# Performance work log

Hardware: AMD Instinct MI355X
Metric: run time of the kernel (lower is better)

## Reference

```python
import jax, jax.numpy as jnp
import numpy as np

N_EMBED = 1024
N_HEADS = 16
CTX = 2048
B, T = 4, 2048
HD = N_EMBED // N_HEADS


def setup_inputs() -> dict:
    key = jax.random.key(0)
    ks = jax.random.split(key, 5)
    scale = 1.0 / np.sqrt(N_EMBED)
    return {
        "x": jax.random.normal(ks[0], (B, T, N_EMBED), dtype=jnp.float32),
        "wq": jax.random.normal(ks[1], (N_EMBED, N_EMBED), dtype=jnp.float32) * scale,
        "wk": jax.random.normal(ks[2], (N_EMBED, N_EMBED), dtype=jnp.float32) * scale,
        "wv": jax.random.normal(ks[3], (N_EMBED, N_EMBED), dtype=jnp.float32) * scale,
        "wo": jax.random.normal(ks[4], (N_EMBED, N_EMBED), dtype=jnp.float32) * scale,
    }


def reference(x, wq, wk, wv, wo):
    b, t, c = x.shape
    # nn.Linear applies x @ W.T ; split heads -> [B, H, T, hd]
    def proj(w):
        return jnp.einsum("btc,dc->btd", x, w).reshape(b, t, N_HEADS, HD).transpose(0, 2, 1, 3)
    q, k, v = proj(wq), proj(wk), proj(wv)
    scores = jnp.einsum("bhqd,bhkd->bhqk", q, k) * (HD ** -0.5)
    causal = jnp.tril(jnp.ones((t, t), dtype=bool))
    scores = jnp.where(causal[None, None, :, :], scores, -jnp.inf)
    a = jax.nn.softmax(scores, axis=-1)
    o = jnp.einsum("bhqk,bhkd->bhqd", a, v)  # [B,H,T,hd]
    o = o.transpose(0, 2, 1, 3).reshape(b, t, c)
    return jnp.einsum("btc,dc->btd", o, wo)
```

## Files before the change

kernel.cpp:

```cpp
#include <hip/hip_runtime.h>
#include <stdint.h>


typedef __attribute__((ext_vector_type(8))) short bf16x8;
typedef __attribute__((ext_vector_type(4))) float f32x4;
typedef __attribute__((ext_vector_type(16))) float f32x16;
typedef unsigned short us;
typedef unsigned int u32;

#define LOG2E 1.4426950408889634f

#define GL2LDS16(g, l)                                                          \
  __builtin_amdgcn_global_load_lds(                                             \
      (const __attribute__((address_space(1))) unsigned int*)(g),               \
      (__attribute__((address_space(3))) unsigned int*)(l), 16, 0, 0)

__device__ inline us f2bf(float f) {
  union { float f; unsigned int u; } v; v.f = f;
  unsigned int u = v.u;
  u += 0x7FFFu + ((u >> 16) & 1u);
  return (us)(u >> 16);
}

__global__ void cast_all(const float* __restrict__ x,
                         const float* __restrict__ w0, const float* __restrict__ w1,
                         const float* __restrict__ w2, const float* __restrict__ w3,
                         us* __restrict__ xb, us* __restrict__ wbuf) {
  int i = (blockIdx.x * blockDim.x + threadIdx.x) * 8;
  const float* src;
  us* dst;
  float sc = 1.0f;
  if (i < (8 << 20)) {
    src = x + i; dst = xb + i;
  } else {
    int j = i - (8 << 20);
    int seg = j >> 20;
    int off = j & ((1 << 20) - 1);
    const float* w = (seg == 0) ? w0 : (seg == 1) ? w1 : (seg == 2) ? w2 : w3;
    if (seg == 0) sc = 0.125f * LOG2E;
    src = w + off; dst = wbuf + j;
  }
  float4 a = *reinterpret_cast<const float4*>(src);
  float4 b = *reinterpret_cast<const float4*>(src + 4);
  union { us u[8]; uint4 v; } o;
  o.u[0] = f2bf(a.x * sc); o.u[1] = f2bf(a.y * sc);
  o.u[2] = f2bf(a.z * sc); o.u[3] = f2bf(a.w * sc);
  o.u[4] = f2bf(b.x * sc); o.u[5] = f2bf(b.y * sc);
  o.u[6] = f2bf(b.z * sc); o.u[7] = f2bf(b.w * sc);
  *reinterpret_cast<uint4*>(dst) = o.v;
}

__global__ __launch_bounds__(512, 2) void gemm_qkv256(
    const us* __restrict__ A, const us* __restrict__ Bw,
    us* __restrict__ QKV, us* __restrict__ Vt) {
  const int K = 1024, N = 3072;
  __shared__ __align__(16) us As[4][8192];
  __shared__ __align__(16) us Bs[4][8192];
  const int tid = threadIdx.x;
  const int lane = tid & 63;
  const int w = tid >> 6;
  const int wm = w >> 2, wn = w & 3;
  const int quad = lane >> 4, l16 = lane & 15;

  const int bid = blockIdx.x;
  const int swz = (bid & 7) * 48 + (bid >> 3);
  const int mt = swz / 12, nt = swz % 12;
  const int m0 = mt * 256, n0 = nt * 256;

  const int j3 = (tid >> 3) & 7;
  const int upre = (tid & 7) ^ j3;
  const int Rb = ((tid >> 3) << 1) | (upre >> 2);
  const int kof = (upre & 3) * 8;
  const size_t arow0 = (size_t)(m0 + Rb) * K + kof;
  const size_t arow1 = (size_t)(m0 + Rb + 128) * K + kof;
  const size_t brow0 = (size_t)(n0 + Rb) * K + kof;
  const size_t brow1 = (size_t)(n0 + Rb + 128) * K + kof;
  const int wofs = __builtin_amdgcn_readfirstlane(w * 512);

  const int lrow = (l16 >> 1) * 64 +
                   ((((l16 & 1) * 4 + quad) ^ ((l16 >> 1) & 7)) * 8);

  f32x4 acc[8][4] = {};

  auto stage = [&](int ss, int ks) {
    const int sb = ss * 8192;
    GL2LDS16(A + arow0 + ks * 32, &As[0][sb + wofs]);
    GL2LDS16(A + arow1 + ks * 32, &As[0][sb + 4096 + wofs]);
    GL2LDS16(Bw + brow0 + ks * 32, &Bs[0][sb + wofs]);
    GL2LDS16(Bw + brow1 + ks * 32, &Bs[0][sb + 4096 + wofs]);
  };

  stage(0, 0);
  stage(1, 1);
  stage(2, 2);

#pragma unroll 1
  for (int s = 0; s < 32; ++s) {
    if (s < 29) {
      stage((s + 3) & 3, s + 3);
      asm volatile("s_waitcnt vmcnt(12)" ::: "memory");
    } else if (s == 29) {
      asm volatile("s_waitcnt vmcnt(8)" ::: "memory");
    } else if (s == 30) {
      asm volatile("s_waitcnt vmcnt(4)" ::: "memory");
    } else {
      asm volatile("s_waitcnt vmcnt(0)" ::: "memory");
    }
    asm volatile("s_barrier" ::: "memory");

    const int sb = (s & 3) * 8192;
    bf16x8 af[8], bf[4];
#pragma unroll
    for (int mi = 0; mi < 8; ++mi)
      af[mi] = *reinterpret_cast<const bf16x8*>(
          &As[0][sb + wm * 4096 + mi * 512 + lrow]);
#pragma unroll
    for (int ni = 0; ni < 4; ++ni)
      bf[ni] = *reinterpret_cast<const bf16x8*>(
          &Bs[0][sb + wn * 2048 + ni * 512 + lrow]);

    __builtin_amdgcn_s_setprio(1);
#pragma unroll
    for (int mi = 0; mi < 8; ++mi)
#pragma unroll
      for (int ni = 0; ni < 4; ++ni)
        acc[mi][ni] = __builtin_amdgcn_mfma_f32_16x16x32_bf16(af[mi], bf[ni], acc[mi][ni], 0, 0, 0);
    __builtin_amdgcn_s_setprio(0);

    asm volatile("s_barrier" ::: "memory");
  }

  if (n0 < 2048) {
#pragma unroll
    for (int mi = 0; mi < 8; ++mi)
#pragma unroll
      for (int ni = 0; ni < 4; ++ni)
#pragma unroll
        for (int r = 0; r < 4; ++r) {
          int row = m0 + wm * 128 + mi * 16 + quad * 4 + r;
          int col = n0 + wn * 64 + ni * 16 + l16;
          QKV[(size_t)row * N + col] = f2bf(acc[mi][ni][r]);
        }
  } else {
    const int bI = m0 >> 11;
    const int tbase = m0 & 2047;
#pragma unroll
    for (int mi = 0; mi < 8; ++mi)
#pragma unroll
      for (int ni = 0; ni < 4; ++ni)
#pragma unroll
        for (int r = 0; r < 4; ++r) {
          int krow = tbase + wm * 128 + mi * 16 + quad * 4 + r;
          int col = n0 + wn * 64 + ni * 16 + l16;
          int hh = (col - 2048) >> 6;
          int d = col & 63;
          Vt[((size_t)((bI * 16 + hh) * 64 + d)) * 2048 + krow] = f2bf(acc[mi][ni][r]);
        }
  }
}

__global__ __launch_bounds__(256, 2) void gemm_out(
    const us* __restrict__ A, const us* __restrict__ Bw,
    float* __restrict__ Cv, int M, int N, int K) {
  __shared__ __align__(16) us Al[128 * 64];
  __shared__ __align__(16) us Bl[128 * 64];
  const int tid = threadIdx.x;
  const int lane = tid & 63;
  const int w = tid >> 6;
  const int quad = lane >> 4;
  const int l16 = lane & 15;
  const int m0 = blockIdx.y * 128;
  const int n0 = blockIdx.x * 128;
  const int wm = w >> 1, wn = w & 1;
  const int srow_base = w * 8 + (lane >> 3);
  const int sunit = lane & 7;
  f32x4 acc[4][4] = {};

  for (int k0 = 0; k0 < K; k0 += 64) {
    __syncthreads();
#pragma unroll
    for (int it = 0; it < 4; ++it) {
      int row = it * 32 + srow_base;
      int gu = sunit ^ (row & 7);
      int base = __builtin_amdgcn_readfirstlane((it * 256 + w * 64) * 8);
      GL2LDS16(A + (size_t)(m0 + row) * K + k0 + gu * 8, &Al[base]);
      GL2LDS16(Bw + (size_t)(n0 + row) * K + k0 + gu * 8, &Bl[base]);
    }
    __syncthreads();
#pragma unroll
    for (int kk = 0; kk < 2; ++kk) {
      bf16x8 af[4], bfr[4];
#pragma unroll
      for (int mi = 0; mi < 4; ++mi) {
        int row = wm * 64 + mi * 16 + l16;
        af[mi] = *reinterpret_cast<const bf16x8*>(
            &Al[row * 64 + (((kk * 4 + quad) ^ (row & 7)) * 8)]);
      }
#pragma unroll
      for (int ni = 0; ni < 4; ++ni) {
        int row = wn * 64 + ni * 16 + l16;
        bfr[ni] = *reinterpret_cast<const bf16x8*>(
            &Bl[row * 64 + (((kk * 4 + quad) ^ (row & 7)) * 8)]);
      }
#pragma unroll
      for (int mi = 0; mi < 4; ++mi)
#pragma unroll
        for (int ni = 0; ni < 4; ++ni)
          acc[mi][ni] = __builtin_amdgcn_mfma_f32_16x16x32_bf16(af[mi], bfr[ni], acc[mi][ni], 0, 0, 0);
    }
  }

#pragma unroll
  for (int mi = 0; mi < 4; ++mi)
#pragma unroll
    for (int ni = 0; ni < 4; ++ni)
#pragma unroll
      for (int r = 0; r < 4; ++r) {
        int row = m0 + wm * 64 + mi * 16 + quad * 4 + r;
        int col = n0 + wn * 64 + ni * 16 + l16;
        Cv[(size_t)row * N + col] = acc[mi][ni][r];
      }
}

__global__ __launch_bounds__(256, 3) void attn(
    const us* __restrict__ QKV, const us* __restrict__ Vt,
    us* __restrict__ O) {
  __shared__ __align__(16) us Kb[2][64 * 64];
  __shared__ __align__(16) us Vb[2][64 * 64];
  __shared__ float Ls[4][32];
  const int bid = blockIdx.x;
  const int j16 = bid >> 6;
  const int grp = j16 >> 2, pos = j16 & 3;
  const int qt = (grp == 0) ? 15 - pos : (grp == 1) ? pos
               : (grp == 2) ? 11 - pos : 4 + pos;
  const int bh = bid & 63;
  const int b = bh >> 4, h = bh & 15;
  const int q0 = qt * 128;
  const int tid = threadIdx.x, lane = tid & 63, w = tid >> 6;
  const int l31 = lane & 31, hi = lane >> 5;
  const size_t rowbase = (size_t)b * 2048;
  const int qcol = h * 64;
  const int kcol = 1024 + h * 64;
  const int qw = q0 + w * 32;
  const int nT = 2 * qt + 2;

  const int mr = (l31 & 7) ^ ((l31 >> 3) & 3);

  bf16x8 qf[4];
#pragma unroll
  for (int ds = 0; ds < 4; ++ds)
    qf[ds] = *reinterpret_cast<const bf16x8*>(
        &QKV[(rowbase + qw + l31) * 3072 + qcol + ds * 16 + hi * 8]);

  f32x16 oacc[2] = {};
  float psum = 0.f;

  const int rr8 = w * 8 + (lane >> 3);
  const int ms = (rr8 & 7) ^ ((rr8 >> 3) & 3);
  const int uu = lane & 7;
  const int gu = uu ^ ms;

  auto stage = [&](int kt, int buf) {
#pragma unroll
    for (int c = 0; c < 2; ++c) {
      int row = c * 32 + rr8;
      int base = __builtin_amdgcn_readfirstlane((c * 32 + w * 8) * 64);
      GL2LDS16(QKV + (rowbase + kt * 64 + row) * 3072 + kcol + gu * 8,
               &Kb[buf][base]);
      GL2LDS16(Vt + ((size_t)(bh * 64 + row)) * 2048 + kt * 64 + gu * 8,
               &Vb[buf][base]);
    }
  };

  stage(0, 0);

  for (int kt = 0; kt < nT; ++kt) {
    asm volatile("s_waitcnt vmcnt(0)" ::: "memory");
    asm volatile("s_barrier" ::: "memory");
    if (kt + 1 < nT) stage(kt + 1, (kt + 1) & 1);
    const us* Kl = &Kb[kt & 1][0];
    const us* Vl = &Vb[kt & 1][0];

    const int kdiff = qw + 31 - kt * 64;
    if (kdiff < 0) continue;
    const int tmax = (kdiff >= 32) ? 2 : 1;
    const bool do_mask = (kt * 64 + 63) > qw;

#pragma unroll
    for (int t = 0; t < 2; ++t) {
      if (t < tmax) {
        f32x16 s = {};
#pragma unroll
        for (int ds = 0; ds < 4; ++ds) {
          int row = t * 32 + l31;
          bf16x8 kf = *reinterpret_cast<const bf16x8*>(
              &Kl[row * 64 + (((ds * 2 + hi) ^ mr) * 8)]);
          s = __builtin_amdgcn_mfma_f32_32x32x16_bf16(kf, qf[ds], s, 0, 0, 0);
        }

        float p[16];
        if (do_mask) {
#pragma unroll
          for (int r = 0; r < 16; ++r) {
            float e = __builtin_amdgcn_exp2f(s[r]);
            int kg = kt * 64 + t * 32 + (r & 3) + ((r >> 2) << 3) + hi * 4;
            p[r] = (kg <= qw + l31) ? e : 0.f;
            psum += p[r];
          }
        } else {
#pragma unroll
          for (int r = 0; r < 16; ++r) {
            p[r] = __builtin_amdgcn_exp2f(s[r]);
            psum += p[r];
          }
        }

        u32 pk[4][2];
#pragma unroll
        for (int bb = 0; bb < 4; ++bb)
#pragma unroll
          for (int w2 = 0; w2 < 2; ++w2)
            asm("v_cvt_pk_bf16_f32 %0, %1, %2"
                : "=v"(pk[bb][w2])
                : "v"(p[4 * bb + 2 * w2]), "v"(p[4 * bb + 2 * w2 + 1]));

#pragma unroll
        for (int s2 = 0; s2 < 2; ++s2) {
          u32 pa[4];
#pragma unroll
          for (int w2 = 0; w2 < 2; ++w2) {
            u32 a = pk[2 * s2][w2];
            u32 c = pk[2 * s2 + 1][w2];
            asm volatile("v_permlane32_swap_b32 %0, %1" : "+v"(a), "+v"(c));
            pa[w2] = a;
            pa[2 + w2] = c;
          }
          union { u32 u[4]; bf16x8 v; } pu;
          pu.u[0] = pa[0]; pu.u[1] = pa[1]; pu.u[2] = pa[2]; pu.u[3] = pa[3];
          bf16x8 paf = pu.v;
          int ks = t * 2 + s2;
#pragma unroll
          for (int dt = 0; dt < 2; ++dt) {
            int row = dt * 32 + l31;
            bf16x8 vf = *reinterpret_cast<const bf16x8*>(
                &Vl[row * 64 + (((ks * 2 + hi) ^ mr) * 8)]);
            oacc[dt] = __builtin_amdgcn_mfma_f32_32x32x16_bf16(paf, vf, oacc[dt], 0, 0, 0);
          }
        }
      }
    }
  }

  {
    float a = psum, c = psum;
    asm volatile("v_permlane32_swap_b32 %0, %1" : "+v"(a), "+v"(c));
    float invl = 1.0f / (a + c);
    if (!hi) Ls[w][l31] = invl;
    asm volatile("s_waitcnt lgkmcnt(0)" ::: "memory");
  }
  float inv[16];
#pragma unroll
  for (int r = 0; r < 16; ++r)
    inv[r] = Ls[w][(r & 3) + ((r >> 2) << 3) + hi * 4];
#pragma unroll
  for (int dt = 0; dt < 2; ++dt)
#pragma unroll
    for (int r = 0; r < 16; ++r) {
      int qg = qw + (r & 3) + ((r >> 2) << 3) + hi * 4;
      O[(rowbase + qg) * 1024 + qcol + dt * 32 + l31] = f2bf(oacc[dt][r] * inv[r]);
    }
}

extern "C" void kernel_launch(void* const* d_in, const int* in_sizes, int n_in,
                              void* d_out, int out_size, void* d_ws, size_t ws_size,
                              hipStream_t stream) {
  const float* x = (const float*)d_in[0];
  const float* wq = (const float*)d_in[1];
  const float* wk = (const float*)d_in[2];
  const float* wv = (const float*)d_in[3];
  const float* wo = (const float*)d_in[4];

  const int BT = 8192, E = 1024;
  const size_t NX = (size_t)BT * E;
  const size_t NW = (size_t)E * E;

  us* xb = (us*)d_ws;
  us* wbuf = xb + NX;
  us* QKV = wbuf + 4 * NW;
  us* VtB = QKV + (size_t)BT * 3 * E;
  us* Ob = xb;

  cast_all<<<(int)((NX + 4 * NW) / 8 / 256), 256, 0, stream>>>(x, wq, wk, wv, wo, xb, wbuf);

  gemm_qkv256<<<384, 512, 0, stream>>>(xb, wbuf, QKV, VtB);
  attn<<<1024, 256, 0, stream>>>(QKV, VtB, Ob);
  gemm_out<<<dim3(8, 64), 256, 0, stream>>>(Ob, wbuf + 3 * NW, (float*)d_out, BT, E, E);
}
```

Baseline: 244.2 us.

## Retile QKV GEMM to 256x192 tiles with finer-grained phased pipeline

Changes the QKV projection GEMM tile from 256x256 to 256x192, raising the grid from 384 to 512 blocks so the 256-CU device gets an even two waves. The main loop is rewritten as eight macro-expanded phases per 64-wide k step, each loading half the A fragments and interleaving global-to-LDS staging with MFMA work, with only six of eight waves loading B. The aim is to remove wave-quantization tail and overlap loads with compute better. It adds more barriers per k step, lowers per-block arithmetic intensity, and the epilogue now picks per 16-column chunk between the QKV and transposed-V outputs.

```diff
diff --git a/kernel.cpp b/kernel.cpp
--- a/kernel.cpp
+++ b/kernel.cpp
@@ -53,9 +53,8 @@
 __global__ __launch_bounds__(512, 2) void gemm_qkv256(
     const us* __restrict__ A, const us* __restrict__ Bw,
     us* __restrict__ QKV, us* __restrict__ Vt) {
-  const int K = 1024, N = 3072;
   __shared__ __align__(16) us As[4][8192];
-  __shared__ __align__(16) us Bs[4][8192];
+  __shared__ __align__(16) us Bs[4][6144];
   const int tid = threadIdx.x;
   const int lane = tid & 63;
   const int w = tid >> 6;
@@ -63,100 +62,139 @@
   const int quad = lane >> 4, l16 = lane & 15;
 
   const int bid = blockIdx.x;
-  const int swz = (bid & 7) * 48 + (bid >> 3);
-  const int mt = swz / 12, nt = swz % 12;
-  const int m0 = mt * 256, n0 = nt * 256;
+  const int swz = (bid & 7) * 64 + (bid >> 3);
+  const int mt = swz >> 4, nt = swz & 15;
+  const int m0 = mt * 256, n0 = nt * 192;
 
   const int j3 = (tid >> 3) & 7;
   const int upre = (tid & 7) ^ j3;
   const int Rb = ((tid >> 3) << 1) | (upre >> 2);
+  const int bRb = Rb;
   const int kof = (upre & 3) * 8;
-  const size_t arow0 = (size_t)(m0 + Rb) * K + kof;
-  const size_t arow1 = (size_t)(m0 + Rb + 128) * K + kof;
-  const size_t brow0 = (size_t)(n0 + Rb) * K + kof;
-  const size_t brow1 = (size_t)(n0 + Rb + 128) * K + kof;
-  const int wofs = __builtin_amdgcn_readfirstlane(w * 512);
+  const int awb = __builtin_amdgcn_readfirstlane(w * 512);
+  const int bwb = awb;
 
   const int lrow = (l16 >> 1) * 64 +
                    ((((l16 & 1) * 4 + quad) ^ ((l16 >> 1) & 7)) * 8);
-
-  f32x4 acc[8][4] = {};
-
-  auto stage = [&](int ss, int ks) {
-    const int sb = ss * 8192;
-    GL2LDS16(A + arow0 + ks * 32, &As[0][sb + wofs]);
-    GL2LDS16(A + arow1 + ks * 32, &As[0][sb + 4096 + wofs]);
-    GL2LDS16(Bw + brow0 + ks * 32, &Bs[0][sb + wofs]);
-    GL2LDS16(Bw + brow1 + ks * 32, &Bs[0][sb + 4096 + wofs]);
-  };
-
-  stage(0, 0);
-  stage(1, 1);
-  stage(2, 2);
+  const int wm4 = wm * 4096;
+  const int wn1536 = wn * 1536;
+
+  f32x4 acc[8][3] = {};
+  bf16x8 b0, b1, b2;
+
+#define STGA(T, KK)                                                            \
+  {                                                                            \
+    const us* s_ = A + (size_t)(m0 + Rb) * 1024 + (T) * 64 + (KK) * 32 + kof;  \
+    us* d_ = (us*)&As[(((T) & 1) * 2 + (KK))][0];                              \
+    GL2LDS16(s_, d_ + awb);                                                    \
+    GL2LDS16(s_ + 128 * 1024, d_ + awb + 4096);                                \
+  }
+#define STGB(T, KK)                                                            \
+  if (w < 6) {                                                                 \
+    const us* s_ = Bw + (size_t)(n0 + bRb) * 1024 + (T) * 64 + (KK) * 32 + kof;\
+    us* d_ = (us*)&Bs[(((T) & 1) * 2 + (KK))][0];                              \
+    GL2LDS16(s_, d_ + bwb);                                                    \
+    GL2LDS16(s_ + 96 * 1024, d_ + bwb + 3072);                                 \
+  }
+#define VMW_STD                                                                \
+  if (w < 6) { asm volatile("s_waitcnt vmcnt(6)" ::: "memory"); }              \
+  else       { asm volatile("s_waitcnt vmcnt(2)" ::: "memory"); }
+#define VMW_ZERO asm volatile("s_waitcnt vmcnt(0)" ::: "memory");
+
+#define MM(a, b, c) __builtin_amdgcn_mfma_f32_16x16x32_bf16(a, b, c, 0, 0, 0)
+#define RDA(S, MH, J) \
+  (*reinterpret_cast<const bf16x8*>(&As[S][wm4 + (MH) * 2048 + (J) * 512 + lrow]))
+#define RDB(S, N) \
+  (*reinterpret_cast<const bf16x8*>(&Bs[S][wn1536 + (N) * 512 + lrow]))
+
+#define PHASE(P, KK, MH, LOADB, STG, VMW)                                      \
+  {                                                                            \
+    enum { SA_ = (P) * 2 + (KK) };                                             \
+    bf16x8 a0 = RDA(SA_, MH, 0), a1 = RDA(SA_, MH, 1),                         \
+           a2 = RDA(SA_, MH, 2), a3 = RDA(SA_, MH, 3);                         \
+    if (LOADB) { b0 = RDB(SA_, 0); b1 = RDB(SA_, 1); b2 = RDB(SA_, 2); }       \
+    STG;                                                                       \
+    asm volatile("s_barrier" ::: "memory");                                    \
+    asm volatile("s_waitcnt lgkmcnt(0)" ::: "memory");                         \
+    __builtin_amdgcn_sched_barrier(0);                                         \
+    __builtin_amdgcn_s_setprio(1);                                             \
+    acc[(MH)*4+0][0] = MM(a0, b0, acc[(MH)*4+0][0]);                           \
+    acc[(MH)*4+0][1] = MM(a0, b1, acc[(MH)*4+0][1]);                           \
+    acc[(MH)*4+0][2] = MM(a0, b2, acc[(MH)*4+0][2]);                           \
+    acc[(MH)*4+1][0] = MM(a1, b0, acc[(MH)*4+1][0]);                           \
+    acc[(MH)*4+1][1] = MM(a1, b1, acc[(MH)*4+1][1]);                           \
+    acc[(MH)*4+1][2] = MM(a1, b2, acc[(MH)*4+1][2]);                           \
+    acc[(MH)*4+2][0] = MM(a2, b0, acc[(MH)*4+2][0]);                           \
+    acc[(MH)*4+2][1] = MM(a2, b1, acc[(MH)*4+2][1]);                           \
+    acc[(MH)*4+2][2] = MM(a2, b2, acc[(MH)*4+2][2]);                           \
+    acc[(MH)*4+3][0] = MM(a3, b0, acc[(MH)*4+3][0]);                           \
+    acc[(MH)*4+3][1] = MM(a3, b1, acc[(MH)*4+3][1]);                           \
+    acc[(MH)*4+3][2] = MM(a3, b2, acc[(MH)*4+3][2]);                           \
+    __builtin_amdgcn_s_setprio(0);                                             \
+    VMW;                                                                       \
+    asm volatile("s_barrier" ::: "memory");                                    \
+  }
+
+  STGB(0, 0); STGA(0, 0); STGB(0, 1); STGA(0, 1);
+  if (w < 6) { asm volatile("s_waitcnt vmcnt(4)" ::: "memory"); }
+  else       { asm volatile("s_waitcnt vmcnt(2)" ::: "memory"); }
+  STGB(1, 0); STGA(1, 0); STGB(1, 1);
+  if (w < 6) { asm volatile("s_waitcnt vmcnt(6)" ::: "memory"); }
+  else       { asm volatile("s_waitcnt vmcnt(2)" ::: "memory"); }
+  asm volatile("s_barrier" ::: "memory");
 
 #pragma unroll 1
-  for (int s = 0; s < 32; ++s) {
-    if (s < 29) {
-      stage((s + 3) & 3, s + 3);
-      asm volatile("s_waitcnt vmcnt(12)" ::: "memory");
-    } else if (s == 29) {
-      asm volatile("s_waitcnt vmcnt(8)" ::: "memory");
-    } else if (s == 30) {
-      asm volatile("s_waitcnt vmcnt(4)" ::: "memory");
-    } else {
-      asm volatile("s_waitcnt vmcnt(0)" ::: "memory");
-    }
-    asm volatile("s_barrier" ::: "memory");
-
-    const int sb = (s & 3) * 8192;
-    bf16x8 af[8], bf[4];
-#pragma unroll
-    for (int mi = 0; mi < 8; ++mi)
-      af[mi] = *reinterpret_cast<const bf16x8*>(
-          &As[0][sb + wm * 4096 + mi * 512 + lrow]);
-#pragma unroll
-    for (int ni = 0; ni < 4; ++ni)
-      bf[ni] = *reinterpret_cast<const bf16x8*>(
-          &Bs[0][sb + wn * 2048 + ni * 512 + lrow]);
-
-    __builtin_amdgcn_s_setprio(1);
-#pragma unroll
-    for (int mi = 0; mi < 8; ++mi)
-#pragma unroll
-      for (int ni = 0; ni < 4; ++ni)
-        acc[mi][ni] = __builtin_amdgcn_mfma_f32_16x16x32_bf16(af[mi], bf[ni], acc[mi][ni], 0, 0, 0);
-    __builtin_amdgcn_s_setprio(0);
-
-    asm volatile("s_barrier" ::: "memory");
-  }
-
-  if (n0 < 2048) {
-#pragma unroll
-    for (int mi = 0; mi < 8; ++mi)
-#pragma unroll
-      for (int ni = 0; ni < 4; ++ni)
+  for (int i = 0; i < 7; ++i) {
+    const int t1 = 2 * i + 1, u0 = 2 * i + 2, u1 = 2 * i + 3;
+    PHASE(0, 0, 0, 1, STGA(t1, 1), );
+    PHASE(0, 0, 1, 0, STGB(u0, 0), );
+    PHASE(0, 1, 0, 1, STGA(u0, 0), );
+    PHASE(0, 1, 1, 0, STGB(u0, 1), VMW_STD);
+    PHASE(1, 0, 0, 1, STGA(u0, 1), );
+    PHASE(1, 0, 1, 0, STGB(u1, 0), );
+    PHASE(1, 1, 0, 1, STGA(u1, 0), );
+    PHASE(1, 1, 1, 0, STGB(u1, 1), VMW_STD);
+  }
+  PHASE(0, 0, 0, 1, STGA(15, 1), );
+  PHASE(0, 0, 1, 0, , );
+  PHASE(0, 1, 0, 1, , );
+  PHASE(0, 1, 1, 0, , VMW_ZERO);
+  PHASE(1, 0, 0, 1, , );
+  PHASE(1, 0, 1, 0, , );
+  PHASE(1, 1, 0, 1, , );
+  PHASE(1, 1, 1, 0, , );
+
+  const int bI = m0 >> 11;
+  const int tbase = m0 & 2047;
+#pragma unroll
+  for (int mi = 0; mi < 8; ++mi)
+#pragma unroll
+    for (int ni = 0; ni < 3; ++ni) {
+      const int colbase = n0 + wn * 48 + ni * 16;
+      if (colbase < 2048) {
 #pragma unroll
         for (int r = 0; r < 4; ++r) {
           int row = m0 + wm * 128 + mi * 16 + quad * 4 + r;
-          int col = n0 + wn * 64 + ni * 16 + l16;
-          QKV[(size_t)row * N + col] = f2bf(acc[mi][ni][r]);
+          QKV[(size_t)row * 3072 + colbase + l16] = f2bf(acc[mi][ni][r]);
         }
-  } else {
-    const int bI = m0 >> 11;
-    const int tbase = m0 & 2047;
-#pragma unroll
-    for (int mi = 0; mi < 8; ++mi)
-#pragma unroll
-      for (int ni = 0; ni < 4; ++ni)
+      } else {
+        const int hh = (colbase - 2048) >> 6;
+        const int d = (colbase + l16) & 63;
 #pragma unroll
         for (int r = 0; r < 4; ++r) {
           int krow = tbase + wm * 128 + mi * 16 + quad * 4 + r;
-          int col = n0 + wn * 64 + ni * 16 + l16;
-          int hh = (col - 2048) >> 6;
-          int d = col & 63;
           Vt[((size_t)((bI * 16 + hh) * 64 + d)) * 2048 + krow] = f2bf(acc[mi][ni][r]);
         }
-  }
+      }
+    }
+#undef STGA
+#undef STGB
+#undef VMW_STD
+#undef VMW_ZERO
+#undef MM
+#undef RDA
+#undef RDB
+#undef PHASE
 }
 
 __global__ __launch_bounds__(256, 2) void gemm_out(
@@ -392,7 +430,7 @@
 
   cast_all<<<(int)((NX + 4 * NW) / 8 / 256), 256, 0, stream>>>(x, wq, wk, wv, wo, xb, wbuf);
 
-  gemm_qkv256<<<384, 512, 0, stream>>>(xb, wbuf, QKV, VtB);
+  gemm_qkv256<<<512, 512, 0, stream>>>(xb, wbuf, QKV, VtB);
   attn<<<1024, 256, 0, stream>>>(QKV, VtB, Ob);
   gemm_out<<<dim3(8, 64), 256, 0, stream>>>(Ob, wbuf + 3 * NW, (float*)d_out, BT, E, E);
 }
```

After: 229.4 us. -6.1%, faster.
